# Kernel optimization log

Measured on AMD Instinct MI355X. Metric: run time of the kernel, lower is better.

## Reference

```python
import jax, jax.numpy as jnp
import numpy as np

I = 18   # input_size
H = 18   # hidden_size
L = 2    # num_layers
B = 4096
T = 512


def setup_inputs() -> dict:
    key = jax.random.key(0)
    ks = jax.random.split(key, 9)
    s = 1.0 / np.sqrt(H)  # PyTorch LSTM init scale
    inp = {"x": jax.random.normal(ks[0], (B, T, I), dtype=jnp.float32)}
    # Layer 0: input size I; Layer 1: input size H. Gate order i,f,g,o (PyTorch).
    inp["w_ih0"] = jax.random.uniform(ks[1], (4 * H, I), jnp.float32, -s, s)
    inp["w_hh0"] = jax.random.uniform(ks[2], (4 * H, H), jnp.float32, -s, s)
    inp["b_ih0"] = jax.random.uniform(ks[3], (4 * H,), jnp.float32, -s, s)
    inp["b_hh0"] = jax.random.uniform(ks[4], (4 * H,), jnp.float32, -s, s)
    inp["w_ih1"] = jax.random.uniform(ks[5], (4 * H, H), jnp.float32, -s, s)
    inp["w_hh1"] = jax.random.uniform(ks[6], (4 * H, H), jnp.float32, -s, s)
    inp["b_ih1"] = jax.random.uniform(ks[7], (4 * H,), jnp.float32, -s, s)
    inp["b_hh1"] = jax.random.uniform(ks[8], (4 * H,), jnp.float32, -s, s)
    return inp


def _lstm_layer(x_tbd, w_ih, w_hh, b_ih, b_hh):
    # x_tbd: [T, B, D_in]; zero initial (h, c) as in the torch module.
    b = b_ih + b_hh
    # Precompute input projection for all timesteps: [T, B, 4H]
    x_proj = jnp.einsum('tbd,gd->tbg', x_tbd, w_ih) + b
    h0 = jnp.zeros((x_tbd.shape[1], H), x_tbd.dtype)
    c0 = jnp.zeros((x_tbd.shape[1], H), x_tbd.dtype)

    def step(carry, xp):
        h, c = carry
        gates = xp + h @ w_hh.T  # [B, 4H]
        i, f, g, o = jnp.split(gates, 4, axis=-1)
        i = jax.nn.sigmoid(i)
        f = jax.nn.sigmoid(f)
        g = jnp.tanh(g)
        o = jax.nn.sigmoid(o)
        c = f * c + i * g
        h = o * jnp.tanh(c)
        return (h, c), h

    _, hs = jax.lax.scan(step, (h0, c0), x_proj)
    return hs  # [T, B, H]


def reference(x, w_ih0, w_hh0, b_ih0, b_hh0, w_ih1, w_hh1, b_ih1, b_hh1):
    x_tbd = jnp.transpose(x, (1, 0, 2))  # [T, B, I]
    h1 = _lstm_layer(x_tbd, w_ih0, w_hh0, b_ih0, b_hh0)
    h2 = _lstm_layer(h1, w_ih1, w_hh1, b_ih1, b_hh1)
    return jnp.transpose(h2, (1, 0, 2))  # [B, T, H]
```

## Files before the change

### kernel.cpp

```cpp
#include <hip/hip_runtime.h>

#define TT   512
#define HD   18
#define NB   16
#define NTH  256
#define RS   68

typedef _Float16 v8h __attribute__((ext_vector_type(8)));
typedef float    v4f __attribute__((ext_vector_type(4)));

__device__ __forceinline__ float fsig(float x) {
    return __builtin_amdgcn_rcpf(1.0f + __expf(-x));
}


template<int NT>
__device__ __forceinline__ void run_wave(
    int tbase, int isl1, int pfmode, int lane,
    const float* __restrict__ x,
    const float* __restrict__ wih, const float* __restrict__ whh,
    const float* __restrict__ bi,  const float* __restrict__ bh,
    float* __restrict__ out,
    _Float16 (*SH)[NB][RS], size_t b0)
{
    const int rl = lane & 15;
    const int lg = lane >> 4;

    v8h Af[NT][2];
    int hh[NT];
    #pragma unroll
    for (int i = 0; i < NT; ++i) {
        const int row = 16 * (tbase + i) + rl;
        const int h = row >> 2, g = row & 3;
        const int r = g * HD + h;
        #pragma unroll
        for (int s = 0; s < 2; ++s) {
            v8h a;
            #pragma unroll
            for (int j = 0; j < 8; ++j) {
                const int k = 8 * lg + j + 32 * s;
                float v = 0.f;
                if (h < HD) {
                    if (k < HD)            v = wih[r * HD + k];
                    else if (k < 2 * HD)   v = whh[r * HD + (k - HD)];
                    else if (k == 2 * HD)  v = bi[r] + bh[r];
                }
                a[j] = (_Float16)v;
            }
            Af[i][s] = a;
        }
        hh[i] = 4 * (tbase + i) + lg;
    }

    float* op[NT];
    #pragma unroll
    for (int i = 0; i < NT; ++i)
        op[i] = out + (b0 + rl) * (size_t)TT * HD + hh[i];

    int pb[3] = {0,0,0}, pk[3] = {0,0,0}; bool pv[3] = {false,false,false};
    float xpf[3] = {0.f, 0.f, 0.f};
    if (pfmode) {
        int ee[3];
        ee[0] = (pfmode == 1) ? lane       : 128 + lane;
        ee[1] = (pfmode == 1) ? 64 + lane  : 192 + lane;
        ee[2] = (pfmode == 1) ? 256 + lane : 999;
        #pragma unroll
        for (int j = 0; j < 3; ++j) {
            pv[j] = ee[j] < NB * HD;
            pb[j] = pv[j] ? ee[j] / HD : 0;
            pk[j] = pv[j] ? ee[j] % HD : 0;
            if (pv[j])
                xpf[j] = x[(b0 + pb[j]) * (size_t)TT * HD + 3 * HD + pk[j]];
        }
    }

    float cst[NT];
    #pragma unroll
    for (int i = 0; i < NT; ++i) cst[i] = 0.f;

    for (int n = 0; n <= TT; ++n) {
        const bool active = isl1 ? (n < TT) : (n >= 1);
        if (active) {
            const int bufi = isl1 ? (n & 3) : (4 + (n & 1));
            const _Float16* rowp = &SH[bufi][rl][0];
            v8h Bf[2];
            #pragma unroll
            for (int s = 0; s < 2; ++s) {
                union { uint2 u[2]; v8h v; } cv;
                cv.u[0] = *(const uint2*)(rowp + 8 * lg + 32 * s);
                cv.u[1] = *(const uint2*)(rowp + 8 * lg + 32 * s + 4);
                Bf[s] = cv.v;
            }
            const int wb1 = (n + 1) & 3;
            const int wb2 = 4 + ((n + 1) & 1);
            #pragma unroll
            for (int i = 0; i < NT; ++i) {
                v4f acc = {0.f, 0.f, 0.f, 0.f};
                acc = __builtin_amdgcn_mfma_f32_16x16x32_f16(Af[i][0], Bf[0], acc, 0, 0, 0);
                acc = __builtin_amdgcn_mfma_f32_16x16x32_f16(Af[i][1], Bf[1], acc, 0, 0, 0);
                const float gi = fsig(acc[0]);
                const float gf = fsig(acc[1]);
                const float gg = 2.f * fsig(2.f * acc[2]) - 1.f;
                const float go = fsig(acc[3]);
                cst[i] = gf * cst[i] + gi * gg;
                const float th = 2.f * fsig(2.f * cst[i]) - 1.f;
                const float hv = go * th;
                const _Float16 h16 = (_Float16)hv;
                if (hh[i] < HD) {
                    if (isl1) {
                        SH[wb1][rl][HD + hh[i]] = h16;
                        SH[wb2][rl][hh[i]]      = h16;
                    } else {
                        SH[wb2][rl][HD + hh[i]] = h16;
                        op[i][(size_t)(n - 1) * HD] = hv;
                    }
                }
            }
        }
        if (pfmode) {
            if (n + 3 < TT) {
                const int xb = (n + 3) & 3;
                #pragma unroll
                for (int j = 0; j < 3; ++j)
                    if (pv[j]) SH[xb][pb[j]][pk[j]] = (_Float16)xpf[j];
            }
            if (n + 4 < TT) {
                #pragma unroll
                for (int j = 0; j < 3; ++j)
                    if (pv[j]) xpf[j] = x[(b0 + pb[j]) * (size_t)TT * HD
                                          + (size_t)(n + 4) * HD + pk[j]];
            }
        }
        __syncthreads();
    }
}

__global__ __launch_bounds__(NTH) void lstm2_mfma(
    const float* __restrict__ x,
    const float* __restrict__ wih0, const float* __restrict__ whh0,
    const float* __restrict__ bih0, const float* __restrict__ bhh0,
    const float* __restrict__ wih1, const float* __restrict__ whh1,
    const float* __restrict__ bih1, const float* __restrict__ bhh1,
    float* __restrict__ out)
{
    __shared__ __align__(16) _Float16 SH[6][NB][RS];

    const int tid  = threadIdx.x;
    const int wid  = tid >> 6;
    const int lane = tid & 63;
    const size_t b0 = (size_t)blockIdx.x * NB;

    {
        uint* shw = (uint*)&SH[0][0][0];
        for (int i = tid; i < 6 * NB * RS / 2; i += NTH) shw[i] = 0u;
        __syncthreads();
        for (int i = tid; i < 6 * NB; i += NTH)
            SH[i / NB][i % NB][2 * HD] = (_Float16)1.0f;
        for (int i = tid; i < 3 * NB * HD; i += NTH) {
            const int t = i / (NB * HD), r2 = i % (NB * HD);
            const int b = r2 / HD, k = r2 % HD;
            SH[t][b][k] = (_Float16)x[(b0 + b) * (size_t)TT * HD + t * HD + k];
        }
        __syncthreads();
    }

    if      (wid == 0) run_wave<3>(0, 1, 0, lane, x, wih0, whh0, bih0, bhh0, out, SH, b0);
    else if (wid == 1) run_wave<2>(3, 1, 1, lane, x, wih0, whh0, bih0, bhh0, out, SH, b0);
    else if (wid == 2) run_wave<3>(0, 0, 0, lane, x, wih1, whh1, bih1, bhh1, out, SH, b0);
    else               run_wave<2>(3, 0, 2, lane, x, wih1, whh1, bih1, bhh1, out, SH, b0);
}

extern "C" void kernel_launch(void* const* d_in, const int* in_sizes, int n_in,
                              void* d_out, int out_size, void* d_ws, size_t ws_size,
                              hipStream_t stream) {
    const float* x    = (const float*)d_in[0];
    const float* wih0 = (const float*)d_in[1];
    const float* whh0 = (const float*)d_in[2];
    const float* bih0 = (const float*)d_in[3];
    const float* bhh0 = (const float*)d_in[4];
    const float* wih1 = (const float*)d_in[5];
    const float* whh1 = (const float*)d_in[6];
    const float* bih1 = (const float*)d_in[7];
    const float* bhh1 = (const float*)d_in[8];
    float* out = (float*)d_out;
    (void)d_ws; (void)ws_size; (void)in_sizes; (void)n_in; (void)out_size;

    lstm2_mfma<<<dim3(4096 / NB), dim3(NTH), 0, stream>>>(
        x, wih0, whh0, bih0, bhh0, wih1, whh1, bih1, bhh1, out);
}
```

Before: 278.3 us.

## Split LSTM gate tiles across ten waves, one MFMA tile per wave

The block grows from four waves, each handling two or three gate tiles, to ten waves that each own a single 16-row gate tile (five per layer). This shortens the serial per-step critical path within a wave and spreads the x prefetch across all waves with a two-step register lookahead. The cost is more waves per block contending in the per-step __syncthreads barrier, and higher per-block thread counts that may limit how many blocks fit on a CU.

```diff
diff --git a/kernel.cpp b/kernel.cpp
--- a/kernel.cpp
+++ b/kernel.cpp
@@ -3,7 +3,7 @@
 #define TT   512
 #define HD   18
 #define NB   16
-#define NTH  256
+#define NTH  640
 #define RS   68
 
 typedef _Float16 v8h __attribute__((ext_vector_type(8)));
@@ -14,128 +14,7 @@
 }
 
 
-template<int NT>
-__device__ __forceinline__ void run_wave(
-    int tbase, int isl1, int pfmode, int lane,
-    const float* __restrict__ x,
-    const float* __restrict__ wih, const float* __restrict__ whh,
-    const float* __restrict__ bi,  const float* __restrict__ bh,
-    float* __restrict__ out,
-    _Float16 (*SH)[NB][RS], size_t b0)
-{
-    const int rl = lane & 15;
-    const int lg = lane >> 4;
-
-    v8h Af[NT][2];
-    int hh[NT];
-    #pragma unroll
-    for (int i = 0; i < NT; ++i) {
-        const int row = 16 * (tbase + i) + rl;
-        const int h = row >> 2, g = row & 3;
-        const int r = g * HD + h;
-        #pragma unroll
-        for (int s = 0; s < 2; ++s) {
-            v8h a;
-            #pragma unroll
-            for (int j = 0; j < 8; ++j) {
-                const int k = 8 * lg + j + 32 * s;
-                float v = 0.f;
-                if (h < HD) {
-                    if (k < HD)            v = wih[r * HD + k];
-                    else if (k < 2 * HD)   v = whh[r * HD + (k - HD)];
-                    else if (k == 2 * HD)  v = bi[r] + bh[r];
-                }
-                a[j] = (_Float16)v;
-            }
-            Af[i][s] = a;
-        }
-        hh[i] = 4 * (tbase + i) + lg;
-    }
-
-    float* op[NT];
-    #pragma unroll
-    for (int i = 0; i < NT; ++i)
-        op[i] = out + (b0 + rl) * (size_t)TT * HD + hh[i];
-
-    int pb[3] = {0,0,0}, pk[3] = {0,0,0}; bool pv[3] = {false,false,false};
-    float xpf[3] = {0.f, 0.f, 0.f};
-    if (pfmode) {
-        int ee[3];
-        ee[0] = (pfmode == 1) ? lane       : 128 + lane;
-        ee[1] = (pfmode == 1) ? 64 + lane  : 192 + lane;
-        ee[2] = (pfmode == 1) ? 256 + lane : 999;
-        #pragma unroll
-        for (int j = 0; j < 3; ++j) {
-            pv[j] = ee[j] < NB * HD;
-            pb[j] = pv[j] ? ee[j] / HD : 0;
-            pk[j] = pv[j] ? ee[j] % HD : 0;
-            if (pv[j])
-                xpf[j] = x[(b0 + pb[j]) * (size_t)TT * HD + 3 * HD + pk[j]];
-        }
-    }
-
-    float cst[NT];
-    #pragma unroll
-    for (int i = 0; i < NT; ++i) cst[i] = 0.f;
-
-    for (int n = 0; n <= TT; ++n) {
-        const bool active = isl1 ? (n < TT) : (n >= 1);
-        if (active) {
-            const int bufi = isl1 ? (n & 3) : (4 + (n & 1));
-            const _Float16* rowp = &SH[bufi][rl][0];
-            v8h Bf[2];
-            #pragma unroll
-            for (int s = 0; s < 2; ++s) {
-                union { uint2 u[2]; v8h v; } cv;
-                cv.u[0] = *(const uint2*)(rowp + 8 * lg + 32 * s);
-                cv.u[1] = *(const uint2*)(rowp + 8 * lg + 32 * s + 4);
-                Bf[s] = cv.v;
-            }
-            const int wb1 = (n + 1) & 3;
-            const int wb2 = 4 + ((n + 1) & 1);
-            #pragma unroll
-            for (int i = 0; i < NT; ++i) {
-                v4f acc = {0.f, 0.f, 0.f, 0.f};
-                acc = __builtin_amdgcn_mfma_f32_16x16x32_f16(Af[i][0], Bf[0], acc, 0, 0, 0);
-                acc = __builtin_amdgcn_mfma_f32_16x16x32_f16(Af[i][1], Bf[1], acc, 0, 0, 0);
-                const float gi = fsig(acc[0]);
-                const float gf = fsig(acc[1]);
-                const float gg = 2.f * fsig(2.f * acc[2]) - 1.f;
-                const float go = fsig(acc[3]);
-                cst[i] = gf * cst[i] + gi * gg;
-                const float th = 2.f * fsig(2.f * cst[i]) - 1.f;
-                const float hv = go * th;
-                const _Float16 h16 = (_Float16)hv;
-                if (hh[i] < HD) {
-                    if (isl1) {
-                        SH[wb1][rl][HD + hh[i]] = h16;
-                        SH[wb2][rl][hh[i]]      = h16;
-                    } else {
-                        SH[wb2][rl][HD + hh[i]] = h16;
-                        op[i][(size_t)(n - 1) * HD] = hv;
-                    }
-                }
-            }
-        }
-        if (pfmode) {
-            if (n + 3 < TT) {
-                const int xb = (n + 3) & 3;
-                #pragma unroll
-                for (int j = 0; j < 3; ++j)
-                    if (pv[j]) SH[xb][pb[j]][pk[j]] = (_Float16)xpf[j];
-            }
-            if (n + 4 < TT) {
-                #pragma unroll
-                for (int j = 0; j < 3; ++j)
-                    if (pv[j]) xpf[j] = x[(b0 + pb[j]) * (size_t)TT * HD
-                                          + (size_t)(n + 4) * HD + pk[j]];
-            }
-        }
-        __syncthreads();
-    }
-}
-
-__global__ __launch_bounds__(NTH) void lstm2_mfma(
+__global__ __launch_bounds__(NTH) void lstm2_mfma10(
     const float* __restrict__ x,
     const float* __restrict__ wih0, const float* __restrict__ whh0,
     const float* __restrict__ bih0, const float* __restrict__ bhh0,
@@ -161,13 +40,101 @@
             const int b = r2 / HD, k = r2 % HD;
             SH[t][b][k] = (_Float16)x[(b0 + b) * (size_t)TT * HD + t * HD + k];
         }
+    }
+
+    const bool isl1 = (wid < 5);
+    const int  tile = isl1 ? wid : wid - 5;
+    const int  rl   = lane & 15;
+    const int  lg   = lane >> 4;
+    const int  hh   = 4 * tile + lg;
+
+    const float* wih = isl1 ? wih0 : wih1;
+    const float* whh = isl1 ? whh0 : whh1;
+    const float* bi  = isl1 ? bih0 : bih1;
+    const float* bh  = isl1 ? bhh0 : bhh1;
+
+    v8h Af[2];
+    {
+        const int row = 16 * tile + rl;
+        const int h = row >> 2, g = row & 3;
+        const int r = g * HD + h;
+        #pragma unroll
+        for (int s = 0; s < 2; ++s) {
+            v8h a;
+            #pragma unroll
+            for (int j = 0; j < 8; ++j) {
+                const int k = 8 * lg + j + 32 * s;
+                float v = 0.f;
+                if (h < HD) {
+                    if (k < HD)            v = wih[r * HD + k];
+                    else if (k < 2 * HD)   v = whh[r * HD + (k - HD)];
+                    else if (k == 2 * HD)  v = bi[r] + bh[r];
+                }
+                a[j] = (_Float16)v;
+            }
+            Af[s] = a;
+        }
+    }
+
+    float* op = out + (b0 + rl) * (size_t)TT * HD + hh;
+
+    const int  pfe = wid * 32 + lane;
+    const bool pv  = (lane < 32) && (pfe < NB * HD);
+    const int  pb  = pv ? pfe / HD : 0;
+    const int  pk  = pv ? pfe % HD : 0;
+    const float* xpp = x + (b0 + pb) * (size_t)TT * HD + pk;
+    float xh = 0.f, xn2 = 0.f;
+    if (pv) { xh = xpp[3 * HD]; xn2 = xpp[4 * HD]; }
+
+    __syncthreads();
+
+    float cst = 0.f;
+
+    for (int n = 0; n <= TT; ++n) {
+        const bool active = isl1 ? (n < TT) : (n >= 1);
+        if (active) {
+            const int bufi = isl1 ? (n & 3) : (4 + (n & 1));
+            const _Float16* rowp = &SH[bufi][rl][0];
+            v8h Bf[2];
+            #pragma unroll
+            for (int s = 0; s < 2; ++s) {
+                union { uint2 u[2]; v8h v; } cv;
+                cv.u[0] = *(const uint2*)(rowp + 8 * lg + 32 * s);
+                cv.u[1] = *(const uint2*)(rowp + 8 * lg + 32 * s + 4);
+                Bf[s] = cv.v;
+            }
+            v4f acc = {0.f, 0.f, 0.f, 0.f};
+            acc = __builtin_amdgcn_mfma_f32_16x16x32_f16(Af[0], Bf[0], acc, 0, 0, 0);
+            acc = __builtin_amdgcn_mfma_f32_16x16x32_f16(Af[1], Bf[1], acc, 0, 0, 0);
+
+            const float gi = fsig(acc[0]);
+            const float gf = fsig(acc[1]);
+            const float gg = 2.f * fsig(2.f * acc[2]) - 1.f;
+            const float go = fsig(acc[3]);
+            cst = gf * cst + gi * gg;
+            const float th = 2.f * fsig(2.f * cst) - 1.f;
+            const float hv = go * th;
+            const _Float16 h16 = (_Float16)hv;
+
+            const int wb1 = (n + 1) & 3;
+            const int wb2 = 4 + ((n + 1) & 1);
+            if (hh < HD) {
+                if (isl1) {
+                    SH[wb1][rl][HD + hh] = h16;
+                    SH[wb2][rl][hh]      = h16;
+                } else {
+                    SH[wb2][rl][HD + hh] = h16;
+                    op[(size_t)(n - 1) * HD] = hv;
+                }
+            }
+        }
+        if (pv) {
+            if (n + 3 < TT) SH[(n + 3) & 3][pb][pk] = (_Float16)xh;
+            xh = xn2;
+            if (n + 5 < TT) xn2 = xpp[(size_t)(n + 5) * HD];
+        }
         __syncthreads();
     }
-
-    if      (wid == 0) run_wave<3>(0, 1, 0, lane, x, wih0, whh0, bih0, bhh0, out, SH, b0);
-    else if (wid == 1) run_wave<2>(3, 1, 1, lane, x, wih0, whh0, bih0, bhh0, out, SH, b0);
-    else if (wid == 2) run_wave<3>(0, 0, 0, lane, x, wih1, whh1, bih1, bhh1, out, SH, b0);
-    else               run_wave<2>(3, 0, 2, lane, x, wih1, whh1, bih1, bhh1, out, SH, b0);
 }
 
 extern "C" void kernel_launch(void* const* d_in, const int* in_sizes, int n_in,
@@ -185,6 +152,6 @@
     float* out = (float*)d_out;
     (void)d_ws; (void)ws_size; (void)in_sizes; (void)n_in; (void)out_size;
 
-    lstm2_mfma<<<dim3(4096 / NB), dim3(NTH), 0, stream>>>(
+    lstm2_mfma10<<<dim3(4096 / NB), dim3(NTH), 0, stream>>>(
         x, wih0, whh0, bih0, bhh0, wih1, whh1, bih1, bhh1, out);
 }
```

After: 493.0 us. 1.77x slower.
